# Kernel optimization log

Hardware: AMD Instinct MI355X
Metric: run time of the kernel (lower is better)

Reference implementation:

```python
import jax, jax.numpy as jnp
import numpy as np

N, C, H, W, SF = 4, 3, 1024, 1024, 4


def setup_inputs() -> dict:
    key = jax.random.key(0)
    ks = jax.random.split(key, 6)
    z = jax.random.normal(ks[0], (N, C, H, W), dtype=jnp.float32)
    Fk = jax.random.normal(ks[1], (N, C, H, W, 2), dtype=jnp.float32)
    FkC = jax.random.normal(ks[2], (N, C, H, W, 2), dtype=jnp.float32)
    F2k = jax.random.normal(ks[3], (N, C, H, W, 2), dtype=jnp.float32)
    FkCFy = jax.random.normal(ks[4], (N, C, H, W, 2), dtype=jnp.float32)
    # alpha is a positive penalty weight; keep it away from 0 (it divides FX)
    alpha = jax.random.uniform(ks[5], (N, 1, 1, 1), dtype=jnp.float32,
                               minval=0.1, maxval=1.0)
    return {"z": z, "Fk": Fk, "FkC": FkC, "F2k": F2k,
            "FkCFy": FkCFy, "alpha": alpha, "sf": SF}


def _toc(t):
    # [..., 2] real/imag pair (old torch.rfft onesided=False layout) -> complex
    return jax.lax.complex(t[..., 0], t[..., 1])


def _block_mean(a, sf):
    # torch splits() + mean over the sf*sf blocks == mean over an sf-strided
    # block decomposition of the H and W axes (order of blocks is irrelevant
    # under the mean). a: (N, C, H, W) complex -> (N, C, H//sf, W//sf)
    n, c, h, w = a.shape
    return a.reshape(n, c, sf, h // sf, sf, w // sf).mean(axis=(2, 4))


def reference(z, Fk, FkC, F2k, FkCFy, alpha, sf):
    # torch.rfft(x, 2, onesided=False) == full 2-D FFT over last two dims
    FR = _toc(FkCFy) + jnp.fft.fft2(alpha * z)                  # (N,C,H,W) complex
    FBR = _block_mean(_toc(Fk) * FR, sf)                        # (N,C,H/sf,W/sf)
    invW = _block_mean(_toc(F2k), sf)                           # (N,C,H/sf,W/sf)
    invWBR = FBR / (invW + alpha)                               # csum adds alpha to real part
    FCBinvWBR = _toc(FkC) * jnp.tile(invWBR, (1, 1, sf, sf))    # torch .repeat == tile
    FX = (FR - FCBinvWBR) / alpha
    # torch.irfft(FX, 2, onesided=False) == real part of inverse 2-D FFT
    return jnp.real(jnp.fft.ifft2(FX))
```

## Files before the change

### kernel.cpp

```cpp
#include <hip/hip_runtime.h>
#include <cmath>

#define HN 1024
#define NCH 12
#define PI2 6.28318530717958647692f

__device__ __forceinline__ float2 cmul(float2 a, float2 b) {
  return make_float2(a.x * b.x - a.y * b.y, a.x * b.y + a.y * b.x);
}

__device__ __forceinline__ int drev(int k) {
  int r = 0;
#pragma unroll
  for (int i = 0; i < 5; ++i) { r = (r << 2) | (k & 3); k >>= 2; }
  return r;
}

#define RIDX(h) ((h) + ((h) >> 4))
#define TIDX(i) ((i) + ((i) >> 4))
#define EIDX(h, c) ((h) * 17 + (c))

template <bool INV>
__device__ __forceinline__ void bf4(float2& a0, float2& a1, float2& a2, float2& a3,
                                    const float2* tw, int e) {
  float2 t0 = make_float2(a0.x + a2.x, a0.y + a2.y);
  float2 t1 = make_float2(a0.x - a2.x, a0.y - a2.y);
  float2 t2 = make_float2(a1.x + a3.x, a1.y + a3.y);
  float2 t3 = make_float2(a1.x - a3.x, a1.y - a3.y);
  float2 b0 = make_float2(t0.x + t2.x, t0.y + t2.y);
  float2 b2 = make_float2(t0.x - t2.x, t0.y - t2.y);
  float2 b1, b3;
  if (!INV) {
    b1 = make_float2(t1.x + t3.y, t1.y - t3.x);
    b3 = make_float2(t1.x - t3.y, t1.y + t3.x);
  } else {
    b1 = make_float2(t1.x - t3.y, t1.y + t3.x);
    b3 = make_float2(t1.x + t3.y, t1.y - t3.x);
  }
  float2 w1 = tw[e], w2 = tw[2 * e], w3 = tw[3 * e];
  if (INV) { w1.y = -w1.y; w2.y = -w2.y; w3.y = -w3.y; }
  a0 = b0;
  a1 = cmul(b1, w1);
  a2 = cmul(b2, w2);
  a3 = cmul(b3, w3);
}

template <bool INV>
__device__ __forceinline__ void bf4t(float2& a0, float2& a1, float2& a2, float2& a3,
                                     const float2* tw, int e) {
  float2 t0 = make_float2(a0.x + a2.x, a0.y + a2.y);
  float2 t1 = make_float2(a0.x - a2.x, a0.y - a2.y);
  float2 t2 = make_float2(a1.x + a3.x, a1.y + a3.y);
  float2 t3 = make_float2(a1.x - a3.x, a1.y - a3.y);
  float2 b0 = make_float2(t0.x + t2.x, t0.y + t2.y);
  float2 b2 = make_float2(t0.x - t2.x, t0.y - t2.y);
  float2 b1, b3;
  if (!INV) {
    b1 = make_float2(t1.x + t3.y, t1.y - t3.x);
    b3 = make_float2(t1.x - t3.y, t1.y + t3.x);
  } else {
    b1 = make_float2(t1.x - t3.y, t1.y + t3.x);
    b3 = make_float2(t1.x + t3.y, t1.y - t3.x);
  }
  float2 w1 = tw[TIDX(e)], w2 = tw[TIDX(2 * e)], w3 = tw[TIDX(3 * e)];
  if (INV) { w1.y = -w1.y; w2.y = -w2.y; w3.y = -w3.y; }
  a0 = b0;
  a1 = cmul(b1, w1);
  a2 = cmul(b2, w2);
  a3 = cmul(b3, w3);
}

__device__ __forceinline__ void tw_init(float2* tw, int t, int nthr) {
  for (int i = t; i < 768; i += nthr) {
    float s, c;
    sincosf((float)i * (PI2 / 1024.f), &s, &c);
    tw[i] = make_float2(c, -s);
  }
}

__device__ __forceinline__ void tw_init_p(float2* tw, int t, int nthr) {
  for (int i = t; i < 768; i += nthr) {
    float s, c;
    sincosf((float)i * (PI2 / 1024.f), &s, &c);
    tw[TIDX(i)] = make_float2(c, -s);
  }
}

template <bool INV>
__device__ __forceinline__ void fft_row(float2* x, const float2* tw, int t) {
#pragma unroll
  for (int ld = 8; ld >= 0; ld -= 2) {
    __syncthreads();
    const int d = 1 << ld;
    int j = t & (d - 1);
    int p0 = ((t >> ld) << (ld + 2)) | j;
    float2 a0 = x[RIDX(p0)];
    float2 a1 = x[RIDX(p0 + d)];
    float2 a2 = x[RIDX(p0 + 2 * d)];
    float2 a3 = x[RIDX(p0 + 3 * d)];
    bf4<INV>(a0, a1, a2, a3, tw, j << (8 - ld));
    x[RIDX(p0)] = a0;
    x[RIDX(p0 + d)] = a1;
    x[RIDX(p0 + 2 * d)] = a2;
    x[RIDX(p0 + 3 * d)] = a3;
  }
  __syncthreads();
}

template <bool INV>
__device__ __forceinline__ void colfft16(float2 (&r)[16], float2 (&q)[16],
                                         float2* ex, const float2* tw,
                                         int u, int c) {
  const int j2 = u & 3, B = u >> 2;
#pragma unroll
  for (int s = 0; s < 4; ++s)
    bf4t<INV>(r[s], r[s + 4], r[s + 8], r[s + 12], tw, u + (s << 6));
#pragma unroll
  for (int g = 0; g < 4; ++g)
    bf4t<INV>(r[4 * g], r[4 * g + 1], r[4 * g + 2], r[4 * g + 3], tw, u << 2);
#pragma unroll
  for (int it = 0; it < 8; ++it)
    ex[EIDX(u + (it << 6), c)] = r[it];
  __syncthreads();
  if (u < 32) {
#pragma unroll
    for (int m = 0; m < 16; ++m) {
      int hl = (B << 6) + j2 + ((m & 3) << 2) + ((m >> 2) << 4);
      q[m] = ex[EIDX(hl, c)];
    }
  }
  __syncthreads();
#pragma unroll
  for (int it = 8; it < 16; ++it)
    ex[EIDX(u + (it << 6) - 512, c)] = r[it];
  __syncthreads();
  if (u >= 32) {
#pragma unroll
    for (int m = 0; m < 16; ++m) {
      int hl = ((B - 8) << 6) + j2 + ((m & 3) << 2) + ((m >> 2) << 4);
      q[m] = ex[EIDX(hl, c)];
    }
  }
#pragma unroll
  for (int a = 0; a < 4; ++a)
    bf4t<INV>(q[a], q[4 + a], q[8 + a], q[12 + a], tw, (j2 + 4 * a) << 4);
#pragma unroll
  for (int b_ = 0; b_ < 4; ++b_)
    bf4t<INV>(q[4 * b_], q[4 * b_ + 1], q[4 * b_ + 2], q[4 * b_ + 3], tw, j2 << 6);
#pragma unroll
  for (int m = 0; m < 16; ++m) {
    float2 v = q[m];
    float2 p;
    p.x = __shfl_xor(v.x, 32);
    p.y = __shfl_xor(v.y, 32);
    float2 w;
    if (j2 & 2) { w.x = p.x - v.x; w.y = p.y - v.y; }
    else        { w.x = v.x + p.x; w.y = v.y + p.y; }
    float2 p2;
    p2.x = __shfl_xor(w.x, 16);
    p2.y = __shfl_xor(w.y, 16);
    float2 o;
    if (j2 == 0)      { o = make_float2(w.x + p2.x, w.y + p2.y); }
    else if (j2 == 1) { o = make_float2(p2.x - w.x, p2.y - w.y); }
    else if (j2 == 2) { o = INV ? make_float2(w.x - p2.y, w.y + p2.x)
                                : make_float2(w.x + p2.y, w.y - p2.x); }
    else              { o = INV ? make_float2(p2.x + w.y, p2.y - w.x)
                                : make_float2(p2.x - w.y, p2.y + w.x); }
    q[m] = o;
  }
}

__global__ __launch_bounds__(256) void k1_rowfft(const float* __restrict__ z,
                                                 const float* __restrict__ alpha,
                                                 float2* __restrict__ A) {
  __shared__ float2 x[1088];
  __shared__ float2 tw[768];
  const int t = threadIdx.x;
  const int row = blockIdx.x, nc = blockIdx.y;
  tw_init(tw, t, 256);
  const float al = alpha[nc / 3];
  const float* zr = z + ((size_t)nc * HN + row) * HN;
#pragma unroll
  for (int it = 0; it < 4; ++it) {
    int h = t + (it << 8);
    x[RIDX(h)] = make_float2(zr[h] * al, 0.f);
  }
  fft_row<false>(x, tw, t);
  float2* Ar = A + ((size_t)nc * HN + row) * HN;
#pragma unroll
  for (int it = 0; it < 4; ++it) {
    int k = t + (it << 8);
    Ar[k] = x[RIDX(drev(k))];
  }
}

__global__ __launch_bounds__(1024, 4) void k2_colfft(float2* __restrict__ A,
                                                     const float2* __restrict__ FkCFy) {
  __shared__ float2 ex[8704];
  __shared__ float2 tw[816];
  const int t = threadIdx.x;
  const int c = t & 15, u = t >> 4;
  const int w0 = blockIdx.x << 4;
  const int nc = blockIdx.y;
  const size_t base = (size_t)nc * HN * HN + w0 + c;
  float2 r[16], q[16];
#pragma unroll
  for (int it = 0; it < 16; ++it)
    r[it] = A[base + (size_t)(u + (it << 6)) * HN];
  tw_init_p(tw, t, 1024);
  __syncthreads();
  colfft16<false>(r, q, ex, tw, u, c);
  const int j2 = u & 3, B = u >> 2;
  const int f = ((j2 & 1) << 1) | (j2 >> 1);
#pragma unroll
  for (int m = 0; m < 16; ++m) {
    int k = (f << 8) | ((m & 3) << 6) | ((m >> 2) << 4) | ((B & 3) << 2) | (B >> 2);
    size_t gi = base + (size_t)k * HN;
    float2 fy = FkCFy[gi];
    A[gi] = make_float2(q[m].x + fy.x, q[m].y + fy.y);
  }
}

__global__ __launch_bounds__(256) void k3_reduce(const float2* __restrict__ A,
                                                 const float2* __restrict__ Fk,
                                                 const float2* __restrict__ F2k,
                                                 const float* __restrict__ alpha,
                                                 float2* __restrict__ iw) {
  int idx = blockIdx.x * 256 + threadIdx.x;
  int j = idx & 255, i = (idx >> 8) & 255, nc = idx >> 16;
  size_t base = (size_t)nc * HN * HN;
  float sx = 0.f, sy = 0.f, wx = 0.f, wy = 0.f;
#pragma unroll
  for (int s1 = 0; s1 < 4; ++s1) {
#pragma unroll
    for (int s2 = 0; s2 < 4; ++s2) {
      size_t gi = base + (size_t)((s1 << 8) + i) * HN + ((s2 << 8) + j);
      float2 fr = A[gi];
      float2 fk = Fk[gi];
      float2 f2 = F2k[gi];
      sx += fk.x * fr.x - fk.y * fr.y;
      sy += fk.x * fr.y + fk.y * fr.x;
      wx += f2.x;
      wy += f2.y;
    }
  }
  const float al = alpha[nc / 3];
  float dx = wx * 0.0625f + al, dy = wy * 0.0625f;
  float nx = sx * 0.0625f, ny = sy * 0.0625f;
  float inv = 1.0f / (dx * dx + dy * dy);
  iw[idx] = make_float2((nx * dx + ny * dy) * inv, (ny * dx - nx * dy) * inv);
}

__global__ __launch_bounds__(1024, 4) void k4_colifft(float2* __restrict__ A,
                                                      const float2* __restrict__ FkC,
                                                      const float2* __restrict__ iw,
                                                      const float* __restrict__ alpha) {
  __shared__ float2 ex[8704];
  __shared__ float2 tw[816];
  const int t = threadIdx.x;
  const int c = t & 15, u = t >> 4;
  const int w0 = blockIdx.x << 4;
  const int nc = blockIdx.y;
  const float ra = 1.0f / alpha[nc / 3];
  const size_t base = (size_t)nc * HN * HN + w0 + c;
  const int jcol = (w0 + c) & 255;
  const float2* iwp = iw + ((size_t)nc << 16);
  float2 r[16], q[16];
#pragma unroll
  for (int it = 0; it < 16; ++it) {
    int h = u + (it << 6);
    size_t gi = base + (size_t)h * HN;
    float2 fr = A[gi];
    float2 fc = FkC[gi];
    float2 w = iwp[((h & 255) << 8) | jcol];
    float2 p = cmul(fc, w);
    r[it] = make_float2((fr.x - p.x) * ra, (fr.y - p.y) * ra);
  }
  tw_init_p(tw, t, 1024);
  __syncthreads();
  colfft16<true>(r, q, ex, tw, u, c);
  const int j2 = u & 3, B = u >> 2;
  const int f = ((j2 & 1) << 1) | (j2 >> 1);
#pragma unroll
  for (int m = 0; m < 16; ++m) {
    int k = (f << 8) | ((m & 3) << 6) | ((m >> 2) << 4) | ((B & 3) << 2) | (B >> 2);
    A[base + (size_t)k * HN] = q[m];
  }
}

__global__ __launch_bounds__(256) void k5_rowifft(const float2* __restrict__ A,
                                                  float* __restrict__ out) {
  __shared__ float2 x[1088];
  __shared__ float2 tw[768];
  const int t = threadIdx.x;
  const int row = blockIdx.x, nc = blockIdx.y;
  tw_init(tw, t, 256);
  const float2* Ar = A + ((size_t)nc * HN + row) * HN;
#pragma unroll
  for (int it = 0; it < 4; ++it) {
    int h = t + (it << 8);
    x[RIDX(h)] = Ar[h];
  }
  fft_row<true>(x, tw, t);
  float* outr = out + ((size_t)nc * HN + row) * HN;
  const float sc = 1.0f / (1024.0f * 1024.0f);
#pragma unroll
  for (int it = 0; it < 4; ++it) {
    int k = t + (it << 8);
    outr[k] = x[RIDX(drev(k))].x * sc;
  }
}

extern "C" void kernel_launch(void* const* d_in, const int* in_sizes, int n_in,
                              void* d_out, int out_size, void* d_ws, size_t ws_size,
                              hipStream_t stream) {
  const float*  z      = (const float*)d_in[0];
  const float2* Fk     = (const float2*)d_in[1];
  const float2* FkC    = (const float2*)d_in[2];
  const float2* F2k    = (const float2*)d_in[3];
  const float2* FkCFy  = (const float2*)d_in[4];
  const float*  alpha  = (const float*)d_in[5];
  (void)in_sizes; (void)n_in; (void)out_size; (void)ws_size;

  float2* A  = (float2*)d_ws;
  float2* iw = A + (size_t)NCH * HN * HN;
  float*  out = (float*)d_out;

  k1_rowfft<<<dim3(HN, NCH), dim3(256), 0, stream>>>(z, alpha, A);
  k2_colfft<<<dim3(HN / 16, NCH), dim3(1024), 0, stream>>>(A, FkCFy);
  k3_reduce<<<dim3(NCH * 256), dim3(256), 0, stream>>>(A, Fk, F2k, alpha, iw);
  k4_colifft<<<dim3(HN / 16, NCH), dim3(1024), 0, stream>>>(A, FkC, iw, alpha);
  k5_rowifft<<<dim3(HN, NCH), dim3(256), 0, stream>>>(A, out);
}
```

Baseline: 279.0 us.

## Fuse block-mean reductions into FFT kernels via atomics and drop reduce kernel

Removes the separate reduction kernel. The F2k block sums are accumulated with float atomics in the row-FFT kernel. The Fk*FR block sums are formed in the column-FFT kernel, using wavefront shuffles across the four frequency blocks followed by atomics. The inverse-weight division moves into the inverse column kernel, which reads the accumulated sums. This avoids re-reading the large intermediate A and one kernel launch, at the cost of a memset of the accumulator buffer, atomic traffic, and non-deterministic float summation order.

```diff
diff --git a/kernel.cpp b/kernel.cpp
--- a/kernel.cpp
+++ b/kernel.cpp
@@ -172,7 +172,9 @@
 
 __global__ __launch_bounds__(256) void k1_rowfft(const float* __restrict__ z,
                                                  const float* __restrict__ alpha,
-                                                 float2* __restrict__ A) {
+                                                 const float2* __restrict__ F2k,
+                                                 float2* __restrict__ A,
+                                                 float4* __restrict__ S) {
   __shared__ float2 x[1088];
   __shared__ float2 tw[768];
   const int t = threadIdx.x;
@@ -185,6 +187,18 @@
     int h = t + (it << 8);
     x[RIDX(h)] = make_float2(zr[h] * al, 0.f);
   }
+  const float2* f2r = F2k + ((size_t)nc * HN + row) * HN;
+  float sxr = 0.f, syr = 0.f;
+#pragma unroll
+  for (int it = 0; it < 4; ++it) {
+    float2 v = f2r[t + (it << 8)];
+    sxr += v.x; syr += v.y;
+  }
+  {
+    float4* sp = S + (((size_t)nc << 16) | ((row & 255) << 8) | t);
+    unsafeAtomicAdd(&sp->z, sxr);
+    unsafeAtomicAdd(&sp->w, syr);
+  }
   fft_row<false>(x, tw, t);
   float2* Ar = A + ((size_t)nc * HN + row) * HN;
 #pragma unroll
@@ -195,7 +209,9 @@
 }
 
 __global__ __launch_bounds__(1024, 4) void k2_colfft(float2* __restrict__ A,
-                                                     const float2* __restrict__ FkCFy) {
+                                                     const float2* __restrict__ FkCFy,
+                                                     const float2* __restrict__ Fk,
+                                                     float4* __restrict__ S) {
   __shared__ float2 ex[8704];
   __shared__ float2 tw[816];
   const int t = threadIdx.x;
@@ -212,48 +228,33 @@
   colfft16<false>(r, q, ex, tw, u, c);
   const int j2 = u & 3, B = u >> 2;
   const int f = ((j2 & 1) << 1) | (j2 >> 1);
+  const int jcol = (w0 + c) & 255;
+  const size_t sbase = ((size_t)nc << 16) | jcol;
 #pragma unroll
   for (int m = 0; m < 16; ++m) {
-    int k = (f << 8) | ((m & 3) << 6) | ((m >> 2) << 4) | ((B & 3) << 2) | (B >> 2);
+    int klo = ((m & 3) << 6) | ((m >> 2) << 4) | ((B & 3) << 2) | (B >> 2);
+    int k = (f << 8) | klo;
     size_t gi = base + (size_t)k * HN;
     float2 fy = FkCFy[gi];
-    A[gi] = make_float2(q[m].x + fy.x, q[m].y + fy.y);
-  }
-}
-
-__global__ __launch_bounds__(256) void k3_reduce(const float2* __restrict__ A,
-                                                 const float2* __restrict__ Fk,
-                                                 const float2* __restrict__ F2k,
-                                                 const float* __restrict__ alpha,
-                                                 float2* __restrict__ iw) {
-  int idx = blockIdx.x * 256 + threadIdx.x;
-  int j = idx & 255, i = (idx >> 8) & 255, nc = idx >> 16;
-  size_t base = (size_t)nc * HN * HN;
-  float sx = 0.f, sy = 0.f, wx = 0.f, wy = 0.f;
-#pragma unroll
-  for (int s1 = 0; s1 < 4; ++s1) {
-#pragma unroll
-    for (int s2 = 0; s2 < 4; ++s2) {
-      size_t gi = base + (size_t)((s1 << 8) + i) * HN + ((s2 << 8) + j);
-      float2 fr = A[gi];
-      float2 fk = Fk[gi];
-      float2 f2 = F2k[gi];
-      sx += fk.x * fr.x - fk.y * fr.y;
-      sy += fk.x * fr.y + fk.y * fr.x;
-      wx += f2.x;
-      wy += f2.y;
+    float2 fr = make_float2(q[m].x + fy.x, q[m].y + fy.y);
+    A[gi] = fr;
+    float2 fk = Fk[gi];
+    float2 pr = cmul(fk, fr);
+    pr.x += __shfl_xor(pr.x, 16);
+    pr.y += __shfl_xor(pr.y, 16);
+    pr.x += __shfl_xor(pr.x, 32);
+    pr.y += __shfl_xor(pr.y, 32);
+    if (j2 == 0) {
+      float4* sp = S + (sbase | (klo << 8));
+      unsafeAtomicAdd(&sp->x, pr.x);
+      unsafeAtomicAdd(&sp->y, pr.y);
     }
   }
-  const float al = alpha[nc / 3];
-  float dx = wx * 0.0625f + al, dy = wy * 0.0625f;
-  float nx = sx * 0.0625f, ny = sy * 0.0625f;
-  float inv = 1.0f / (dx * dx + dy * dy);
-  iw[idx] = make_float2((nx * dx + ny * dy) * inv, (ny * dx - nx * dy) * inv);
 }
 
 __global__ __launch_bounds__(1024, 4) void k4_colifft(float2* __restrict__ A,
                                                       const float2* __restrict__ FkC,
-                                                      const float2* __restrict__ iw,
+                                                      const float4* __restrict__ S,
                                                       const float* __restrict__ alpha) {
   __shared__ float2 ex[8704];
   __shared__ float2 tw[816];
@@ -261,10 +262,11 @@
   const int c = t & 15, u = t >> 4;
   const int w0 = blockIdx.x << 4;
   const int nc = blockIdx.y;
-  const float ra = 1.0f / alpha[nc / 3];
+  const float al = alpha[nc / 3];
+  const float ra = 1.0f / al;
   const size_t base = (size_t)nc * HN * HN + w0 + c;
   const int jcol = (w0 + c) & 255;
-  const float2* iwp = iw + ((size_t)nc << 16);
+  const float4* Sp = S + ((size_t)nc << 16);
   float2 r[16], q[16];
 #pragma unroll
   for (int it = 0; it < 16; ++it) {
@@ -272,7 +274,11 @@
     size_t gi = base + (size_t)h * HN;
     float2 fr = A[gi];
     float2 fc = FkC[gi];
-    float2 w = iwp[((h & 255) << 8) | jcol];
+    float4 sv = Sp[((h & 255) << 8) | jcol];
+    float dx = sv.z * 0.0625f + al, dy = sv.w * 0.0625f;
+    float nx = sv.x * 0.0625f, ny = sv.y * 0.0625f;
+    float invd = 1.0f / (dx * dx + dy * dy);
+    float2 w = make_float2((nx * dx + ny * dy) * invd, (ny * dx - nx * dy) * invd);
     float2 p = cmul(fc, w);
     r[it] = make_float2((fr.x - p.x) * ra, (fr.y - p.y) * ra);
   }
@@ -322,13 +328,14 @@
   const float*  alpha  = (const float*)d_in[5];
   (void)in_sizes; (void)n_in; (void)out_size; (void)ws_size;
 
-  float2* A  = (float2*)d_ws;
-  float2* iw = A + (size_t)NCH * HN * HN;
+  float2* A = (float2*)d_ws;
+  float4* S = (float4*)((char*)d_ws + (size_t)NCH * HN * HN * sizeof(float2));
   float*  out = (float*)d_out;
 
-  k1_rowfft<<<dim3(HN, NCH), dim3(256), 0, stream>>>(z, alpha, A);
-  k2_colfft<<<dim3(HN / 16, NCH), dim3(1024), 0, stream>>>(A, FkCFy);
-  k3_reduce<<<dim3(NCH * 256), dim3(256), 0, stream>>>(A, Fk, F2k, alpha, iw);
-  k4_colifft<<<dim3(HN / 16, NCH), dim3(1024), 0, stream>>>(A, FkC, iw, alpha);
+  hipMemsetAsync(S, 0, (size_t)NCH * 256 * 256 * sizeof(float4), stream);
+
+  k1_rowfft<<<dim3(HN, NCH), dim3(256), 0, stream>>>(z, alpha, F2k, A, S);
+  k2_colfft<<<dim3(HN / 16, NCH), dim3(1024), 0, stream>>>(A, FkCFy, Fk, S);
+  k4_colifft<<<dim3(HN / 16, NCH), dim3(1024), 0, stream>>>(A, FkC, S, alpha);
   k5_rowifft<<<dim3(HN, NCH), dim3(256), 0, stream>>>(A, out);
 }
```

Result: slower. 379.8 us (+36.1%).

## Run row FFTs one wavefront per row with register radix-16 and shuffles

Applied to the files above, without the earlier changes.

Row FFT kernels now map each 1024-point row to a single 64-lane wavefront. The wavefront holds 16 values per lane in registers and exchanges data through a private LDS slice and cross-lane shuffles, replacing five block-wide barrier-separated radix-4 passes. Eight rows share a 512-thread block along with one twiddle table. The column kernels also hoist the FkCFy loads ahead of the FFT and reuse the four distinct iw values per thread instead of reloading them. This relies on wave-synchronous LDS ordering enforced only by s_waitcnt rather than barriers, which assumes 64-wide wavefronts.

```diff
diff --git a/kernel.cpp b/kernel.cpp
--- a/kernel.cpp
+++ b/kernel.cpp
@@ -9,41 +9,9 @@
   return make_float2(a.x * b.x - a.y * b.y, a.x * b.y + a.y * b.x);
 }
 
-__device__ __forceinline__ int drev(int k) {
-  int r = 0;
-#pragma unroll
-  for (int i = 0; i < 5; ++i) { r = (r << 2) | (k & 3); k >>= 2; }
-  return r;
-}
-
-#define RIDX(h) ((h) + ((h) >> 4))
 #define TIDX(i) ((i) + ((i) >> 4))
 #define EIDX(h, c) ((h) * 17 + (c))
-
-template <bool INV>
-__device__ __forceinline__ void bf4(float2& a0, float2& a1, float2& a2, float2& a3,
-                                    const float2* tw, int e) {
-  float2 t0 = make_float2(a0.x + a2.x, a0.y + a2.y);
-  float2 t1 = make_float2(a0.x - a2.x, a0.y - a2.y);
-  float2 t2 = make_float2(a1.x + a3.x, a1.y + a3.y);
-  float2 t3 = make_float2(a1.x - a3.x, a1.y - a3.y);
-  float2 b0 = make_float2(t0.x + t2.x, t0.y + t2.y);
-  float2 b2 = make_float2(t0.x - t2.x, t0.y - t2.y);
-  float2 b1, b3;
-  if (!INV) {
-    b1 = make_float2(t1.x + t3.y, t1.y - t3.x);
-    b3 = make_float2(t1.x - t3.y, t1.y + t3.x);
-  } else {
-    b1 = make_float2(t1.x - t3.y, t1.y + t3.x);
-    b3 = make_float2(t1.x + t3.y, t1.y - t3.x);
-  }
-  float2 w1 = tw[e], w2 = tw[2 * e], w3 = tw[3 * e];
-  if (INV) { w1.y = -w1.y; w2.y = -w2.y; w3.y = -w3.y; }
-  a0 = b0;
-  a1 = cmul(b1, w1);
-  a2 = cmul(b2, w2);
-  a3 = cmul(b3, w3);
-}
+#define WIDX(h) ((h) + ((h) >> 4))
 
 template <bool INV>
 __device__ __forceinline__ void bf4t(float2& a0, float2& a1, float2& a2, float2& a3,
@@ -70,14 +38,6 @@
   a3 = cmul(b3, w3);
 }
 
-__device__ __forceinline__ void tw_init(float2* tw, int t, int nthr) {
-  for (int i = t; i < 768; i += nthr) {
-    float s, c;
-    sincosf((float)i * (PI2 / 1024.f), &s, &c);
-    tw[i] = make_float2(c, -s);
-  }
-}
-
 __device__ __forceinline__ void tw_init_p(float2* tw, int t, int nthr) {
   for (int i = t; i < 768; i += nthr) {
     float s, c;
@@ -87,24 +47,49 @@
 }
 
 template <bool INV>
-__device__ __forceinline__ void fft_row(float2* x, const float2* tw, int t) {
-#pragma unroll
-  for (int ld = 8; ld >= 0; ld -= 2) {
-    __syncthreads();
-    const int d = 1 << ld;
-    int j = t & (d - 1);
-    int p0 = ((t >> ld) << (ld + 2)) | j;
-    float2 a0 = x[RIDX(p0)];
-    float2 a1 = x[RIDX(p0 + d)];
-    float2 a2 = x[RIDX(p0 + 2 * d)];
-    float2 a3 = x[RIDX(p0 + 3 * d)];
-    bf4<INV>(a0, a1, a2, a3, tw, j << (8 - ld));
-    x[RIDX(p0)] = a0;
-    x[RIDX(p0 + d)] = a1;
-    x[RIDX(p0 + 2 * d)] = a2;
-    x[RIDX(p0 + 3 * d)] = a3;
-  }
-  __syncthreads();
+__device__ __forceinline__ void wavefft16(float2 (&r)[16], float2 (&q)[16],
+                                          float2* ex, const float2* tw, int u) {
+  const int j2 = u & 3, B = u >> 2;
+#pragma unroll
+  for (int s = 0; s < 4; ++s)
+    bf4t<INV>(r[s], r[s + 4], r[s + 8], r[s + 12], tw, u + (s << 6));
+#pragma unroll
+  for (int g = 0; g < 4; ++g)
+    bf4t<INV>(r[4 * g], r[4 * g + 1], r[4 * g + 2], r[4 * g + 3], tw, u << 2);
+#pragma unroll
+  for (int it = 0; it < 16; ++it)
+    ex[WIDX(u + (it << 6))] = r[it];
+  asm volatile("s_waitcnt lgkmcnt(0)" ::: "memory");
+#pragma unroll
+  for (int m = 0; m < 16; ++m)
+    q[m] = ex[WIDX((B << 6) + j2 + ((m & 3) << 2) + ((m >> 2) << 4))];
+#pragma unroll
+  for (int a = 0; a < 4; ++a)
+    bf4t<INV>(q[a], q[4 + a], q[8 + a], q[12 + a], tw, (j2 + 4 * a) << 4);
+#pragma unroll
+  for (int b_ = 0; b_ < 4; ++b_)
+    bf4t<INV>(q[4 * b_], q[4 * b_ + 1], q[4 * b_ + 2], q[4 * b_ + 3], tw, j2 << 6);
+#pragma unroll
+  for (int m = 0; m < 16; ++m) {
+    float2 v = q[m];
+    float2 p;
+    p.x = __shfl_xor(v.x, 2);
+    p.y = __shfl_xor(v.y, 2);
+    float2 w;
+    if (j2 & 2) { w.x = p.x - v.x; w.y = p.y - v.y; }
+    else        { w.x = v.x + p.x; w.y = v.y + p.y; }
+    float2 p2;
+    p2.x = __shfl_xor(w.x, 1);
+    p2.y = __shfl_xor(w.y, 1);
+    float2 o;
+    if (j2 == 0)      { o = make_float2(w.x + p2.x, w.y + p2.y); }
+    else if (j2 == 1) { o = make_float2(p2.x - w.x, p2.y - w.y); }
+    else if (j2 == 2) { o = INV ? make_float2(w.x - p2.y, w.y + p2.x)
+                                : make_float2(w.x + p2.y, w.y - p2.x); }
+    else              { o = INV ? make_float2(p2.x + w.y, p2.y - w.x)
+                                : make_float2(p2.x - w.y, p2.y + w.x); }
+    q[m] = o;
+  }
 }
 
 template <bool INV>
@@ -170,27 +155,37 @@
   }
 }
 
-__global__ __launch_bounds__(256) void k1_rowfft(const float* __restrict__ z,
+__global__ __launch_bounds__(512) void k1_rowfft(const float* __restrict__ z,
                                                  const float* __restrict__ alpha,
                                                  float2* __restrict__ A) {
-  __shared__ float2 x[1088];
-  __shared__ float2 tw[768];
+  __shared__ float2 ex[8 * 1088];
+  __shared__ float2 tw[816];
   const int t = threadIdx.x;
-  const int row = blockIdx.x, nc = blockIdx.y;
-  tw_init(tw, t, 256);
+  const int w = t >> 6, u = t & 63;
+  const int row = (blockIdx.x << 3) + w, nc = blockIdx.y;
+  tw_init_p(tw, t, 512);
+  __syncthreads();
   const float al = alpha[nc / 3];
   const float* zr = z + ((size_t)nc * HN + row) * HN;
-#pragma unroll
-  for (int it = 0; it < 4; ++it) {
-    int h = t + (it << 8);
-    x[RIDX(h)] = make_float2(zr[h] * al, 0.f);
-  }
-  fft_row<false>(x, tw, t);
+  float2 r[16], q[16];
+#pragma unroll
+  for (int it = 0; it < 16; ++it)
+    r[it] = make_float2(zr[u + (it << 6)] * al, 0.f);
+  float2* exw = ex + w * 1088;
+  wavefft16<false>(r, q, exw, tw, u);
+  const int j2 = u & 3, B = u >> 2;
+  const int f = ((j2 & 1) << 1) | (j2 >> 1);
+#pragma unroll
+  for (int m = 0; m < 16; ++m) {
+    int k = (f << 8) | ((m & 3) << 6) | ((m >> 2) << 4) | ((B & 3) << 2) | (B >> 2);
+    exw[WIDX(k)] = q[m];
+  }
+  asm volatile("s_waitcnt lgkmcnt(0)" ::: "memory");
   float2* Ar = A + ((size_t)nc * HN + row) * HN;
 #pragma unroll
-  for (int it = 0; it < 4; ++it) {
-    int k = t + (it << 8);
-    Ar[k] = x[RIDX(drev(k))];
+  for (int it = 0; it < 16; ++it) {
+    int k = u + (it << 6);
+    Ar[k] = exw[WIDX(k)];
   }
 }
 
@@ -202,22 +197,26 @@
   const int c = t & 15, u = t >> 4;
   const int w0 = blockIdx.x << 4;
   const int nc = blockIdx.y;
+  tw_init_p(tw, t, 1024);
+  __syncthreads();
   const size_t base = (size_t)nc * HN * HN + w0 + c;
-  float2 r[16], q[16];
+  const int j2 = u & 3, B = u >> 2;
+  const int f = ((j2 & 1) << 1) | (j2 >> 1);
+  float2 r[16], fy[16];
 #pragma unroll
   for (int it = 0; it < 16; ++it)
     r[it] = A[base + (size_t)(u + (it << 6)) * HN];
-  tw_init_p(tw, t, 1024);
-  __syncthreads();
+#pragma unroll
+  for (int m = 0; m < 16; ++m) {
+    int k = (f << 8) | ((m & 3) << 6) | ((m >> 2) << 4) | ((B & 3) << 2) | (B >> 2);
+    fy[m] = FkCFy[base + (size_t)k * HN];
+  }
+  float2 q[16];
   colfft16<false>(r, q, ex, tw, u, c);
-  const int j2 = u & 3, B = u >> 2;
-  const int f = ((j2 & 1) << 1) | (j2 >> 1);
-#pragma unroll
-  for (int m = 0; m < 16; ++m) {
-    int k = (f << 8) | ((m & 3) << 6) | ((m >> 2) << 4) | ((B & 3) << 2) | (B >> 2);
-    size_t gi = base + (size_t)k * HN;
-    float2 fy = FkCFy[gi];
-    A[gi] = make_float2(q[m].x + fy.x, q[m].y + fy.y);
+#pragma unroll
+  for (int m = 0; m < 16; ++m) {
+    int k = (f << 8) | ((m & 3) << 6) | ((m >> 2) << 4) | ((B & 3) << 2) | (B >> 2);
+    A[base + (size_t)k * HN] = make_float2(q[m].x + fy[m].x, q[m].y + fy[m].y);
   }
 }
 
@@ -261,10 +260,17 @@
   const int c = t & 15, u = t >> 4;
   const int w0 = blockIdx.x << 4;
   const int nc = blockIdx.y;
-  const float ra = 1.0f / alpha[nc / 3];
+  tw_init_p(tw, t, 1024);
+  __syncthreads();
+  const float al = alpha[nc / 3];
+  const float ra = 1.0f / al;
   const size_t base = (size_t)nc * HN * HN + w0 + c;
   const int jcol = (w0 + c) & 255;
   const float2* iwp = iw + ((size_t)nc << 16);
+  float2 wv[4];
+#pragma unroll
+  for (int s = 0; s < 4; ++s)
+    wv[s] = iwp[((u + (s << 6)) << 8) | jcol];
   float2 r[16], q[16];
 #pragma unroll
   for (int it = 0; it < 16; ++it) {
@@ -272,12 +278,9 @@
     size_t gi = base + (size_t)h * HN;
     float2 fr = A[gi];
     float2 fc = FkC[gi];
-    float2 w = iwp[((h & 255) << 8) | jcol];
-    float2 p = cmul(fc, w);
+    float2 p = cmul(fc, wv[it & 3]);
     r[it] = make_float2((fr.x - p.x) * ra, (fr.y - p.y) * ra);
   }
-  tw_init_p(tw, t, 1024);
-  __syncthreads();
   colfft16<true>(r, q, ex, tw, u, c);
   const int j2 = u & 3, B = u >> 2;
   const int f = ((j2 & 1) << 1) | (j2 >> 1);
@@ -288,26 +291,36 @@
   }
 }
 
-__global__ __launch_bounds__(256) void k5_rowifft(const float2* __restrict__ A,
+__global__ __launch_bounds__(512) void k5_rowifft(const float2* __restrict__ A,
                                                   float* __restrict__ out) {
-  __shared__ float2 x[1088];
-  __shared__ float2 tw[768];
+  __shared__ float2 ex[8 * 1088];
+  __shared__ float2 tw[816];
   const int t = threadIdx.x;
-  const int row = blockIdx.x, nc = blockIdx.y;
-  tw_init(tw, t, 256);
+  const int w = t >> 6, u = t & 63;
+  const int row = (blockIdx.x << 3) + w, nc = blockIdx.y;
+  tw_init_p(tw, t, 512);
+  __syncthreads();
   const float2* Ar = A + ((size_t)nc * HN + row) * HN;
-#pragma unroll
-  for (int it = 0; it < 4; ++it) {
-    int h = t + (it << 8);
-    x[RIDX(h)] = Ar[h];
-  }
-  fft_row<true>(x, tw, t);
+  float2 r[16], q[16];
+#pragma unroll
+  for (int it = 0; it < 16; ++it)
+    r[it] = Ar[u + (it << 6)];
+  float2* exw = ex + w * 1088;
+  wavefft16<true>(r, q, exw, tw, u);
+  const int j2 = u & 3, B = u >> 2;
+  const int f = ((j2 & 1) << 1) | (j2 >> 1);
+#pragma unroll
+  for (int m = 0; m < 16; ++m) {
+    int k = (f << 8) | ((m & 3) << 6) | ((m >> 2) << 4) | ((B & 3) << 2) | (B >> 2);
+    exw[WIDX(k)] = q[m];
+  }
+  asm volatile("s_waitcnt lgkmcnt(0)" ::: "memory");
   float* outr = out + ((size_t)nc * HN + row) * HN;
   const float sc = 1.0f / (1024.0f * 1024.0f);
 #pragma unroll
-  for (int it = 0; it < 4; ++it) {
-    int k = t + (it << 8);
-    outr[k] = x[RIDX(drev(k))].x * sc;
+  for (int it = 0; it < 16; ++it) {
+    int k = u + (it << 6);
+    outr[k] = exw[WIDX(k)].x * sc;
   }
 }
 
@@ -326,9 +339,9 @@
   float2* iw = A + (size_t)NCH * HN * HN;
   float*  out = (float*)d_out;
 
-  k1_rowfft<<<dim3(HN, NCH), dim3(256), 0, stream>>>(z, alpha, A);
+  k1_rowfft<<<dim3(HN / 8, NCH), dim3(512), 0, stream>>>(z, alpha, A);
   k2_colfft<<<dim3(HN / 16, NCH), dim3(1024), 0, stream>>>(A, FkCFy);
   k3_reduce<<<dim3(NCH * 256), dim3(256), 0, stream>>>(A, Fk, F2k, alpha, iw);
   k4_colifft<<<dim3(HN / 16, NCH), dim3(1024), 0, stream>>>(A, FkC, iw, alpha);
-  k5_rowifft<<<dim3(HN, NCH), dim3(256), 0, stream>>>(A, out);
-}
+  k5_rowifft<<<dim3(HN / 8, NCH), dim3(512), 0, stream>>>(A, out);
+}
```

Result: slower. 349.5 us (+25.3%).

## XOR-swizzle intermediate array columns by row to spread column-FFT accesses across channels

Applied to the files above, without the earlier changes.

Stores the intermediate spectrum A with a row-dependent XOR swizzle of 16-column groups, and every kernel that reads or writes A uses the swizzled index. The column-FFT kernels read 16-wide strips at a 1024-element stride, which likely concentrates traffic on a few memory channels or cache sets. The swizzle is meant to spread those strided accesses. Row kernels still access whole rows contiguously, but k3 now reads A in a scattered pattern, and every A access pays a little extra index arithmetic.

```diff
diff --git a/kernel.cpp b/kernel.cpp
--- a/kernel.cpp
+++ b/kernel.cpp
@@ -15,6 +15,8 @@
   for (int i = 0; i < 5; ++i) { r = (r << 2) | (k & 3); k >>= 2; }
   return r;
 }
+
+__device__ __forceinline__ int aswz(int h, int w) { return w ^ ((h & 63) << 4); }
 
 #define RIDX(h) ((h) + ((h) >> 4))
 #define TIDX(i) ((i) + ((i) >> 4))
@@ -186,11 +188,12 @@
     x[RIDX(h)] = make_float2(zr[h] * al, 0.f);
   }
   fft_row<false>(x, tw, t);
-  float2* Ar = A + ((size_t)nc * HN + row) * HN;
+  float2* Ar = A + (size_t)nc * HN * HN + (size_t)row * HN;
+  const int X = (row & 63) << 4;
 #pragma unroll
   for (int it = 0; it < 4; ++it) {
     int k = t + (it << 8);
-    Ar[k] = x[RIDX(drev(k))];
+    Ar[k ^ X] = x[RIDX(drev(k))];
   }
 }
 
@@ -202,11 +205,13 @@
   const int c = t & 15, u = t >> 4;
   const int w0 = blockIdx.x << 4;
   const int nc = blockIdx.y;
-  const size_t base = (size_t)nc * HN * HN + w0 + c;
+  const size_t base = (size_t)nc * HN * HN;
   float2 r[16], q[16];
 #pragma unroll
-  for (int it = 0; it < 16; ++it)
-    r[it] = A[base + (size_t)(u + (it << 6)) * HN];
+  for (int it = 0; it < 16; ++it) {
+    int h = u + (it << 6);
+    r[it] = A[base + (size_t)h * HN + (aswz(h, w0) + c)];
+  }
   tw_init_p(tw, t, 1024);
   __syncthreads();
   colfft16<false>(r, q, ex, tw, u, c);
@@ -215,9 +220,9 @@
 #pragma unroll
   for (int m = 0; m < 16; ++m) {
     int k = (f << 8) | ((m & 3) << 6) | ((m >> 2) << 4) | ((B & 3) << 2) | (B >> 2);
-    size_t gi = base + (size_t)k * HN;
-    float2 fy = FkCFy[gi];
-    A[gi] = make_float2(q[m].x + fy.x, q[m].y + fy.y);
+    float2 fy = FkCFy[base + (size_t)k * HN + w0 + c];
+    A[base + (size_t)k * HN + (aswz(k, w0) + c)] =
+        make_float2(q[m].x + fy.x, q[m].y + fy.y);
   }
 }
 
@@ -234,10 +239,11 @@
   for (int s1 = 0; s1 < 4; ++s1) {
 #pragma unroll
     for (int s2 = 0; s2 < 4; ++s2) {
-      size_t gi = base + (size_t)((s1 << 8) + i) * HN + ((s2 << 8) + j);
-      float2 fr = A[gi];
-      float2 fk = Fk[gi];
-      float2 f2 = F2k[gi];
+      int h = (s1 << 8) + i, w = (s2 << 8) + j;
+      size_t gl = base + (size_t)h * HN + w;
+      float2 fr = A[base + (size_t)h * HN + aswz(h, w)];
+      float2 fk = Fk[gl];
+      float2 f2 = F2k[gl];
       sx += fk.x * fr.x - fk.y * fr.y;
       sy += fk.x * fr.y + fk.y * fr.x;
       wx += f2.x;
@@ -261,17 +267,17 @@
   const int c = t & 15, u = t >> 4;
   const int w0 = blockIdx.x << 4;
   const int nc = blockIdx.y;
-  const float ra = 1.0f / alpha[nc / 3];
-  const size_t base = (size_t)nc * HN * HN + w0 + c;
+  const float al = alpha[nc / 3];
+  const float ra = 1.0f / al;
+  const size_t base = (size_t)nc * HN * HN;
   const int jcol = (w0 + c) & 255;
   const float2* iwp = iw + ((size_t)nc << 16);
   float2 r[16], q[16];
 #pragma unroll
   for (int it = 0; it < 16; ++it) {
     int h = u + (it << 6);
-    size_t gi = base + (size_t)h * HN;
-    float2 fr = A[gi];
-    float2 fc = FkC[gi];
+    float2 fr = A[base + (size_t)h * HN + (aswz(h, w0) + c)];
+    float2 fc = FkC[base + (size_t)h * HN + w0 + c];
     float2 w = iwp[((h & 255) << 8) | jcol];
     float2 p = cmul(fc, w);
     r[it] = make_float2((fr.x - p.x) * ra, (fr.y - p.y) * ra);
@@ -284,7 +290,7 @@
 #pragma unroll
   for (int m = 0; m < 16; ++m) {
     int k = (f << 8) | ((m & 3) << 6) | ((m >> 2) << 4) | ((B & 3) << 2) | (B >> 2);
-    A[base + (size_t)k * HN] = q[m];
+    A[base + (size_t)k * HN + (aswz(k, w0) + c)] = q[m];
   }
 }
 
@@ -295,11 +301,12 @@
   const int t = threadIdx.x;
   const int row = blockIdx.x, nc = blockIdx.y;
   tw_init(tw, t, 256);
-  const float2* Ar = A + ((size_t)nc * HN + row) * HN;
+  const float2* Ar = A + (size_t)nc * HN * HN + (size_t)row * HN;
+  const int X = (row & 63) << 4;
 #pragma unroll
   for (int it = 0; it < 4; ++it) {
     int h = t + (it << 8);
-    x[RIDX(h)] = Ar[h];
+    x[RIDX(h)] = Ar[h ^ X];
   }
   fft_row<true>(x, tw, t);
   float* outr = out + ((size_t)nc * HN + row) * HN;
```

Measured after the change: 278.1 us. Within noise of the previous version (-0.3%).
